# Optimization experiments

Hardware: AMD Instinct MI355X
Metric: run time of the kernel (lower is better)

## Reference

```python
import jax, jax.numpy as jnp
import numpy as np

N_NODES = 50000
N_EDGES = 800000
VOCAB = 500
IN_DIM = 128
HID = 128
OUT_DIM = 64
N_GRAPHS = 512


def setup_inputs() -> dict:
    key = jax.random.key(0)
    ks = jax.random.split(key, 12)
    s = 0.05
    return {
        "emb": jax.random.normal(ks[0], (VOCAB, IN_DIM), jnp.float32) * s,
        "w1a": jax.random.normal(ks[1], (HID, IN_DIM), jnp.float32) * s,
        "b1a": jnp.zeros((HID,), jnp.float32),
        "w1b": jax.random.normal(ks[2], (HID, HID), jnp.float32) * s,
        "b1b": jnp.zeros((HID,), jnp.float32),
        "w2a": jax.random.normal(ks[3], (HID, HID), jnp.float32) * s,
        "b2a": jnp.zeros((HID,), jnp.float32),
        "w2b": jax.random.normal(ks[4], (HID, HID), jnp.float32) * s,
        "b2b": jnp.zeros((HID,), jnp.float32),
        "fc_w": jax.random.normal(ks[5], (OUT_DIM, HID), jnp.float32) * s,
        "fc_b": jnp.zeros((OUT_DIM,), jnp.float32),
        "x_idx": jax.random.randint(ks[6], (N_NODES,), 0, VOCAB, jnp.int32),
        "edge_index": jax.random.randint(ks[7], (2, N_EDGES), 0, N_NODES, jnp.int32),
        "batch": jnp.sort(jax.random.randint(ks[8], (N_NODES,), 0, N_GRAPHS, jnp.int32)),
    }


def gin_conv(x, wa, ba, wb, bb, src, dst):
    # GINConv with eps=0: MLP(x + sum_{j->i} x_j)
    agg = jax.ops.segment_sum(x[src], dst, num_segments=N_NODES)  # [N, d]
    h = x + agg
    h = jax.nn.relu(h @ wa.T + ba)
    return h @ wb.T + bb


def reference(emb, w1a, b1a, w1b, b1b, w2a, b2a, w2b, b2b, fc_w, fc_b,
              x_idx, edge_index, batch):
    src, dst = edge_index[0], edge_index[1]
    x = emb[x_idx]  # [N, IN_DIM] embedding lookup
    x = jax.nn.relu(gin_conv(x, w1a, b1a, w1b, b1b, src, dst))
    x = jax.nn.relu(gin_conv(x, w2a, b2a, w2b, b2b, src, dst))
    # global mean pool over graphs
    sums = jax.ops.segment_sum(x, batch, num_segments=N_GRAPHS)  # [G, HID]
    cnt = jax.ops.segment_sum(jnp.ones((N_NODES,), x.dtype), batch, num_segments=N_GRAPHS)
    pooled = sums / jnp.maximum(cnt, 1.0)[:, None]
    return pooled @ fc_w.T + fc_b  # [G, OUT_DIM]
```

## Files before the change

kernel.cpp:

```cpp
#include <hip/hip_runtime.h>

#define N_NODES 50000
#define N_EDGES 800000
#define DIM 128
#define NGRAPH 512
#define ODIM 64
#define VOCAB 500
#define NBKT 391
#define NB2 128
#define EPB2 (N_EDGES / NB2)
#define CAP 4096

typedef __attribute__((ext_vector_type(8))) short bf16x8;
typedef __attribute__((ext_vector_type(4))) short bf16x4;
typedef __attribute__((ext_vector_type(4))) float f32x4;

__device__ inline unsigned short f2bf(float f) {
  unsigned u = __builtin_bit_cast(unsigned, f);
  return (unsigned short)((u + 0x7fffu + ((u >> 16) & 1u)) >> 16);
}
__device__ inline float bf2f(unsigned short h) {
  unsigned u = ((unsigned)h) << 16;
  return __builtin_bit_cast(float, u);
}

__global__ __launch_bounds__(256) void prep_kernel(
    const float* __restrict__ emb,
    const float* __restrict__ w1a, const float* __restrict__ w1b,
    const float* __restrict__ w2a, const float* __restrict__ w2b,
    unsigned short* __restrict__ embb, unsigned short* __restrict__ wbf,
    int* __restrict__ gcnt) {
  int u = blockIdx.x * 256 + threadIdx.x;
  if (u < NBKT) gcnt[u] = 0;
  const float* src;
  unsigned short* dst;
  if (u < VOCAB * 16) {
    src = emb + (size_t)u * 8;
    dst = embb + (size_t)u * 8;
  } else {
    int v = u - VOCAB * 16;
    if (v >= 4 * 2048) return;
    int m = v >> 11, loc = v & 2047;
    const float* w = (m == 0) ? w1a : (m == 1) ? w1b : (m == 2) ? w2a : w2b;
    src = w + (size_t)loc * 8;
    dst = wbf + (size_t)v * 8;
  }
  f32x4 a = ((const f32x4*)src)[0], b = ((const f32x4*)src)[1];
  bf16x8 o;
  #pragma unroll
  for (int e = 0; e < 4; ++e) {
    o[e] = (short)f2bf(a[e]);
    o[4 + e] = (short)f2bf(b[e]);
  }
  *(bf16x8*)dst = o;
}

__global__ __launch_bounds__(512) void build_kernel(
    const int* __restrict__ ei, int* __restrict__ gcnt,
    unsigned* __restrict__ eb) {
  __shared__ unsigned cnt[NBKT];
  __shared__ unsigned base[NBKT];
  int t = threadIdx.x, b = blockIdx.x;
  for (int i = t; i < NBKT; i += 512) cnt[i] = 0;
  __syncthreads();
  int ebase = b * EPB2;
  for (int i = t; i < EPB2; i += 512)
    atomicAdd(&cnt[(unsigned)ei[N_EDGES + ebase + i] >> 7], 1u);
  __syncthreads();
  for (int i = t; i < NBKT; i += 512) {
    base[i] = (unsigned)atomicAdd(&gcnt[i], (int)cnt[i]);
    cnt[i] = 0;
  }
  __syncthreads();
  for (int i = t; i < EPB2; i += 512) {
    int sn = ei[ebase + i];
    unsigned d = (unsigned)ei[N_EDGES + ebase + i];
    unsigned bk = d >> 7;
    unsigned r = atomicAdd(&cnt[bk], 1u);
    unsigned pos = base[bk] + r;
    if (pos < CAP)
      eb[(size_t)bk * CAP + pos] = ((d & 127u) << 16) | (unsigned)sn;
  }
}

__global__ __launch_bounds__(512) void sort_agg1_kernel(
    const unsigned* __restrict__ eb, const int* __restrict__ gcnt,
    const unsigned short* __restrict__ embb, const int* __restrict__ xidx,
    unsigned short* __restrict__ srt16, int* __restrict__ rowlo,
    int* __restrict__ rowhi, unsigned short* __restrict__ xa) {
  __shared__ unsigned stage[CAP];
  __shared__ unsigned short sorted[CAP];
  __shared__ unsigned hist[128], cur[128];
  __shared__ unsigned wtot;
  int t = threadIdx.x, bkt = blockIdx.x;
  int cnt = gcnt[bkt];
  if (cnt > CAP) cnt = CAP;
  size_t ebbase = (size_t)bkt * CAP;
  if (t < 128) hist[t] = 0;
  __syncthreads();
  for (int i = t; i < cnt; i += 512) {
    unsigned e = eb[ebbase + i];
    stage[i] = e;
    atomicAdd(&hist[e >> 16], 1u);
  }
  __syncthreads();
  if (t < 128) {
    int lane = t & 63;
    unsigned v = hist[t], ss = v;
    #pragma unroll
    for (int d = 1; d < 64; d <<= 1) {
      unsigned u = __shfl_up(ss, d, 64);
      if (lane >= d) ss += u;
    }
    if (t == 63) wtot = ss;
    cur[t] = ss - v;
  }
  __syncthreads();
  if (t < 128) {
    unsigned e0 = cur[t] + (t >= 64 ? wtot : 0u);
    cur[t] = e0;
    int n = bkt * 128 + t;
    if (n < N_NODES) {
      rowlo[n] = (int)(ebbase + e0);
      rowhi[n] = (int)(ebbase + e0 + hist[t]);
    }
  }
  __syncthreads();
  for (int i = t; i < cnt; i += 512) {
    unsigned e = stage[i];
    unsigned r = atomicAdd(&cur[e >> 16], 1u);
    sorted[r] = (unsigned short)(e & 0xFFFFu);
  }
  __syncthreads();

  for (int i = t; i < cnt; i += 512) srt16[ebbase + i] = sorted[i];

  int g = t >> 4, c = t & 15;
  for (int ii = 0; ii < 4; ++ii) {
    int dloc = ii * 32 + g;
    int node = bkt * 128 + dloc;
    if (node >= N_NODES) continue;
    int hi = (int)cur[dloc];
    int lo = hi - (int)hist[dloc];
    bf16x8 sv = *(const bf16x8*)(embb + (size_t)xidx[node] * DIM + c * 8);
    float a[8];
    #pragma unroll
    for (int e = 0; e < 8; ++e) a[e] = bf2f((unsigned short)sv[e]);
    int k = lo;
    for (; k + 8 <= hi; k += 8) {
      bf16x8 w[8];
      #pragma unroll
      for (int q = 0; q < 8; ++q)
        w[q] = *(const bf16x8*)(embb + (size_t)xidx[sorted[k + q]] * DIM + c * 8);
      #pragma unroll
      for (int q = 0; q < 8; ++q)
        #pragma unroll
        for (int e = 0; e < 8; ++e) a[e] += bf2f((unsigned short)w[q][e]);
    }
    for (; k + 2 <= hi; k += 2) {
      bf16x8 w0 = *(const bf16x8*)(embb + (size_t)xidx[sorted[k]] * DIM + c * 8);
      bf16x8 w1 = *(const bf16x8*)(embb + (size_t)xidx[sorted[k + 1]] * DIM + c * 8);
      #pragma unroll
      for (int e = 0; e < 8; ++e)
        a[e] += bf2f((unsigned short)w0[e]) + bf2f((unsigned short)w1[e]);
    }
    if (k < hi) {
      bf16x8 w = *(const bf16x8*)(embb + (size_t)xidx[sorted[k]] * DIM + c * 8);
      #pragma unroll
      for (int e = 0; e < 8; ++e) a[e] += bf2f((unsigned short)w[e]);
    }
    bf16x8 o;
    #pragma unroll
    for (int e = 0; e < 8; ++e) o[e] = (short)f2bf(a[e]);
    *(bf16x8*)(xa + (size_t)node * DIM + c * 8) = o;
  }
}

__global__ __launch_bounds__(256) void agg_x_kernel(
    const unsigned short* __restrict__ x, const int* __restrict__ rowlo,
    const int* __restrict__ rowhi, const unsigned short* __restrict__ srt16,
    unsigned short* __restrict__ xa) {
  int n = blockIdx.x * 16 + (threadIdx.x >> 4);
  int c = threadIdx.x & 15;
  int lo = rowlo[n], hi = rowhi[n];
  bf16x8 sv = *(const bf16x8*)(x + (size_t)n * DIM + c * 8);
  float a[8];
  #pragma unroll
  for (int e = 0; e < 8; ++e) a[e] = bf2f((unsigned short)sv[e]);
  int k = lo;
  for (; k + 8 <= hi; k += 8) {
    bf16x8 w[8];
    #pragma unroll
    for (int q = 0; q < 8; ++q)
      w[q] = *(const bf16x8*)(x + (size_t)srt16[k + q] * DIM + c * 8);
    #pragma unroll
    for (int q = 0; q < 8; ++q)
      #pragma unroll
      for (int e = 0; e < 8; ++e) a[e] += bf2f((unsigned short)w[q][e]);
  }
  for (; k + 2 <= hi; k += 2) {
    bf16x8 w0 = *(const bf16x8*)(x + (size_t)srt16[k] * DIM + c * 8);
    bf16x8 w1 = *(const bf16x8*)(x + (size_t)srt16[k + 1] * DIM + c * 8);
    #pragma unroll
    for (int e = 0; e < 8; ++e)
      a[e] += bf2f((unsigned short)w0[e]) + bf2f((unsigned short)w1[e]);
  }
  if (k < hi) {
    bf16x8 w = *(const bf16x8*)(x + (size_t)srt16[k] * DIM + c * 8);
    #pragma unroll
    for (int e = 0; e < 8; ++e) a[e] += bf2f((unsigned short)w[e]);
  }
  bf16x8 o;
  #pragma unroll
  for (int e = 0; e < 8; ++e) o[e] = (short)f2bf(a[e]);
  *(bf16x8*)(xa + (size_t)n * DIM + c * 8) = o;
}

__global__ __launch_bounds__(256) void mlp_mfma_kernel(
    const unsigned short* __restrict__ xa,
    const unsigned short* __restrict__ wabf, const float* __restrict__ ba,
    const unsigned short* __restrict__ wbbf, const float* __restrict__ bb,
    unsigned short* __restrict__ xout) {
  __shared__ short Xs[64 * 128];
  __shared__ short Hs[64 * 128];
  int t = threadIdx.x;
  int lane = t & 63;
  int w = t >> 6;
  int jq = w * 32;
  int l15 = lane & 15;
  int lg = lane >> 4;

  bf16x8 waf[2][4], wbf[2][4];
  #pragma unroll
  for (int jm = 0; jm < 2; ++jm) {
    int jrow = jq + jm * 16 + l15;
    #pragma unroll
    for (int ks = 0; ks < 4; ++ks) {
      int k0 = ks * 32 + lg * 8;
      waf[jm][ks] = *(const bf16x8*)(wabf + (size_t)jrow * DIM + k0);
      wbf[jm][ks] = *(const bf16x8*)(wbbf + (size_t)jrow * DIM + k0);
    }
  }
  f32x4 ba_r[2], bb_r[2];
  #pragma unroll
  for (int jm = 0; jm < 2; ++jm) {
    ba_r[jm] = *(const f32x4*)(ba + jq + jm * 16 + lg * 4);
    bb_r[jm] = *(const f32x4*)(bb + jq + jm * 16 + lg * 4);
  }

  for (int half = 0; half < 2; ++half) {
    int nbase = blockIdx.x * 128 + half * 64;

    {
      int r = t >> 2;
      int cb = (t & 3) * 4;
      int node = nbase + r;
      #pragma unroll
      for (int i = 0; i < 4; ++i) {
        int chunk = cb + i;
        bf16x8 v = {0, 0, 0, 0, 0, 0, 0, 0};
        if (node < N_NODES)
          v = *(const bf16x8*)(xa + (size_t)node * DIM + chunk * 8);
        *(bf16x8*)&Xs[r * 128 + ((chunk ^ (r & 7)) << 3)] = v;
      }
    }
    __syncthreads();

    #pragma unroll
    for (int nt = 0; nt < 4; ++nt) {
      int rrow = nt * 16 + l15;
      bf16x8 xf[4];
      #pragma unroll
      for (int ks = 0; ks < 4; ++ks) {
        int chunk = ks * 4 + lg;
        xf[ks] = *(const bf16x8*)&Xs[rrow * 128 + ((chunk ^ (rrow & 7)) << 3)];
      }
      #pragma unroll
      for (int jm = 0; jm < 2; ++jm) {
        f32x4 acc = ba_r[jm];
        #pragma unroll
        for (int ks = 0; ks < 4; ++ks)
          acc = __builtin_amdgcn_mfma_f32_16x16x32_bf16(waf[jm][ks], xf[ks], acc, 0, 0, 0);
        int hnode = nt * 16 + l15;
        int cbase = jq + jm * 16 + lg * 4;
        unsigned p0 = (unsigned)f2bf(fmaxf(acc[0], 0.f)) |
                      ((unsigned)f2bf(fmaxf(acc[1], 0.f)) << 16);
        unsigned p1 = (unsigned)f2bf(fmaxf(acc[2], 0.f)) |
                      ((unsigned)f2bf(fmaxf(acc[3], 0.f)) << 16);
        unsigned idx = hnode * 128 + (((cbase >> 3) ^ (hnode & 7)) << 3) + (cbase & 7);
        *(uint2*)&Hs[idx] = make_uint2(p0, p1);
      }
    }
    __syncthreads();

    #pragma unroll
    for (int nt = 0; nt < 4; ++nt) {
      int rrow = nt * 16 + l15;
      bf16x8 hf[4];
      #pragma unroll
      for (int ks = 0; ks < 4; ++ks) {
        int chunk = ks * 4 + lg;
        hf[ks] = *(const bf16x8*)&Hs[rrow * 128 + ((chunk ^ (rrow & 7)) << 3)];
      }
      #pragma unroll
      for (int jm = 0; jm < 2; ++jm) {
        f32x4 acc = bb_r[jm];
        #pragma unroll
        for (int ks = 0; ks < 4; ++ks)
          acc = __builtin_amdgcn_mfma_f32_16x16x32_bf16(wbf[jm][ks], hf[ks], acc, 0, 0, 0);
        int node = nbase + nt * 16 + l15;
        if (node < N_NODES) {
          bf16x4 o;
          #pragma unroll
          for (int e = 0; e < 4; ++e) o[e] = (short)f2bf(fmaxf(acc[e], 0.f));
          *(bf16x4*)(xout + (size_t)node * DIM + jq + jm * 16 + lg * 4) = o;
        }
      }
    }
    __syncthreads();
  }
}

#define PP 132
__global__ __launch_bounds__(256) void pool_fc_kernel(
    const unsigned short* __restrict__ x, const int* __restrict__ batch,
    const float* __restrict__ fcw, const float* __restrict__ fcb,
    float* __restrict__ out) {
  int g = blockIdx.x, t = threadIdx.x;
  __shared__ float part[16 * PP];
  __shared__ float pooled[DIM];
  __shared__ int sbound[2];
  if (t < 2) {
    int target = g + t;
    int lo = 0, hi = N_NODES;
    while (lo < hi) {
      int m = (lo + hi) >> 1;
      if (batch[m] < target) lo = m + 1; else hi = m;
    }
    sbound[t] = lo;
  }
  __syncthreads();
  int lo = sbound[0], hi = sbound[1];
  int r = t >> 4, c = t & 15;
  float acc[8] = {0.f, 0.f, 0.f, 0.f, 0.f, 0.f, 0.f, 0.f};
  for (int nn = lo + r; nn < hi; nn += 16) {
    bf16x8 v = *(const bf16x8*)(x + (size_t)nn * DIM + c * 8);
    #pragma unroll
    for (int e = 0; e < 8; ++e) acc[e] += bf2f((unsigned short)v[e]);
  }
  #pragma unroll
  for (int e = 0; e < 8; ++e) part[r * PP + c * 8 + e] = acc[e];
  __syncthreads();
  if (t < DIM) {
    float s = 0.f;
    #pragma unroll
    for (int rr = 0; rr < 16; ++rr) s += part[rr * PP + t];
    pooled[t] = s / fmaxf((float)(hi - lo), 1.0f);
  }
  __syncthreads();
  if (t < ODIM) {
    float a = fcb[t];
    const float* wr = fcw + (size_t)t * DIM;
    #pragma unroll 8
    for (int h = 0; h < DIM; ++h) a += pooled[h] * wr[h];
    out[(size_t)g * ODIM + t] = a;
  }
}

extern "C" void kernel_launch(void* const* d_in, const int* in_sizes, int n_in,
                              void* d_out, int out_size, void* d_ws, size_t ws_size,
                              hipStream_t stream) {
  const float* emb  = (const float*)d_in[0];
  const float* w1a  = (const float*)d_in[1];
  const float* b1a  = (const float*)d_in[2];
  const float* w1b  = (const float*)d_in[3];
  const float* b1b  = (const float*)d_in[4];
  const float* w2a  = (const float*)d_in[5];
  const float* b2a  = (const float*)d_in[6];
  const float* w2b  = (const float*)d_in[7];
  const float* b2b  = (const float*)d_in[8];
  const float* fcw  = (const float*)d_in[9];
  const float* fcb  = (const float*)d_in[10];
  const int*   xidx = (const int*)d_in[11];
  const int*   ei   = (const int*)d_in[12];
  const int*   batch= (const int*)d_in[13];
  float* out = (float*)d_out;

  size_t featb = (size_t)N_NODES * DIM * sizeof(unsigned short);
  char* ws = (char*)d_ws;
  unsigned short* B1 = (unsigned short*)ws;
  unsigned short* B2 = (unsigned short*)(ws + featb);
  char* p = ws + 2 * featb;
  unsigned short* embb = (unsigned short*)p;  p += (VOCAB * DIM * 2 + 15) / 16 * 16;
  unsigned short* wbf  = (unsigned short*)p;  p += (4 * DIM * DIM * 2 + 15) / 16 * 16;
  int* gcnt  = (int*)p;     p += (NBKT * 4 + 15) / 16 * 16;
  int* rowlo = (int*)p;     p += ((size_t)N_NODES * 4 + 15) / 16 * 16;
  int* rowhi = (int*)p;     p += ((size_t)N_NODES * 4 + 15) / 16 * 16;
  unsigned* eb = (unsigned*)p;          p += (size_t)NBKT * CAP * 4;
  unsigned short* srt16 = (unsigned short*)p;

  const unsigned short* w1abf = wbf;
  const unsigned short* w1bbf = wbf + DIM * DIM;
  const unsigned short* w2abf = wbf + 2 * DIM * DIM;
  const unsigned short* w2bbf = wbf + 3 * DIM * DIM;

  prep_kernel<<<(VOCAB * 16 + 4 * 2048 + 255) / 256, 256, 0, stream>>>(
      emb, w1a, w1b, w2a, w2b, embb, wbf, gcnt);

  build_kernel<<<NB2, 512, 0, stream>>>(ei, gcnt, eb);

  sort_agg1_kernel<<<NBKT, 512, 0, stream>>>(eb, gcnt, embb, xidx, srt16, rowlo, rowhi, B1);
  mlp_mfma_kernel<<<(N_NODES + 127) / 128, 256, 0, stream>>>(B1, w1abf, b1a, w1bbf, b1b, B2);

  agg_x_kernel<<<N_NODES / 16, 256, 0, stream>>>(B2, rowlo, rowhi, srt16, B1);
  mlp_mfma_kernel<<<(N_NODES + 127) / 128, 256, 0, stream>>>(B1, w2abf, b2a, w2bbf, b2b, B2);

  pool_fc_kernel<<<NGRAPH, 256, 0, stream>>>(B2, batch, fcw, fcb, out);
}
```

Measured before the change: 120.6 us.

## Fuse global mean-pool into second MLP kernel and widen sort/agg blocks

The second GIN MLP kernel now writes its ReLU output into shared memory as fp32 and accumulates per-graph column sums straight into a global pooled buffer with atomics. This skips writing and re-reading the final node features, and the pool kernel becomes a small FC kernel that divides by the node count. The sort/aggregate kernel also moves from 512 to 1024 threads per block so each thread handles fewer destination nodes. The cost is float atomics (non-deterministic summation order), a 64KB shared buffer that may lower occupancy, and an extra zeroing pass in prep.

```diff
diff --git a/kernel.cpp b/kernel.cpp
--- a/kernel.cpp
+++ b/kernel.cpp
@@ -29,9 +29,10 @@
     const float* __restrict__ w1a, const float* __restrict__ w1b,
     const float* __restrict__ w2a, const float* __restrict__ w2b,
     unsigned short* __restrict__ embb, unsigned short* __restrict__ wbf,
-    int* __restrict__ gcnt) {
+    int* __restrict__ gcnt, float* __restrict__ pooled) {
   int u = blockIdx.x * 256 + threadIdx.x;
   if (u < NBKT) gcnt[u] = 0;
+  for (int i = u; i < NGRAPH * DIM; i += 64 * 256) pooled[i] = 0.f;
   const float* src;
   unsigned short* dst;
   if (u < VOCAB * 16) {
@@ -83,7 +84,7 @@
   }
 }
 
-__global__ __launch_bounds__(512) void sort_agg1_kernel(
+__global__ __launch_bounds__(1024) void sort_agg1_kernel(
     const unsigned* __restrict__ eb, const int* __restrict__ gcnt,
     const unsigned short* __restrict__ embb, const int* __restrict__ xidx,
     unsigned short* __restrict__ srt16, int* __restrict__ rowlo,
@@ -98,7 +99,7 @@
   size_t ebbase = (size_t)bkt * CAP;
   if (t < 128) hist[t] = 0;
   __syncthreads();
-  for (int i = t; i < cnt; i += 512) {
+  for (int i = t; i < cnt; i += 1024) {
     unsigned e = eb[ebbase + i];
     stage[i] = e;
     atomicAdd(&hist[e >> 16], 1u);
@@ -126,18 +127,18 @@
     }
   }
   __syncthreads();
-  for (int i = t; i < cnt; i += 512) {
+  for (int i = t; i < cnt; i += 1024) {
     unsigned e = stage[i];
     unsigned r = atomicAdd(&cur[e >> 16], 1u);
     sorted[r] = (unsigned short)(e & 0xFFFFu);
   }
   __syncthreads();
 
-  for (int i = t; i < cnt; i += 512) srt16[ebbase + i] = sorted[i];
+  for (int i = t; i < cnt; i += 1024) srt16[ebbase + i] = sorted[i];
 
   int g = t >> 4, c = t & 15;
-  for (int ii = 0; ii < 4; ++ii) {
-    int dloc = ii * 32 + g;
+  for (int ii = 0; ii < 2; ++ii) {
+    int dloc = ii * 64 + g;
     int node = bkt * 128 + dloc;
     if (node >= N_NODES) continue;
     int hi = (int)cur[dloc];
@@ -216,13 +217,17 @@
   *(bf16x8*)(xa + (size_t)n * DIM + c * 8) = o;
 }
 
+template <int POOL>
 __global__ __launch_bounds__(256) void mlp_mfma_kernel(
     const unsigned short* __restrict__ xa,
     const unsigned short* __restrict__ wabf, const float* __restrict__ ba,
     const unsigned short* __restrict__ wbbf, const float* __restrict__ bb,
-    unsigned short* __restrict__ xout) {
-  __shared__ short Xs[64 * 128];
-  __shared__ short Hs[64 * 128];
+    unsigned short* __restrict__ xout, const int* __restrict__ batch,
+    float* __restrict__ pooled) {
+  __shared__ char smem[65536];
+  short* Xs = (short*)smem;
+  short* Hs = (short*)(smem + 32768);
+  float* Fs = (float*)smem;
   int t = threadIdx.x;
   int lane = t & 63;
   int w = t >> 6;
@@ -266,6 +271,7 @@
     }
     __syncthreads();
 
+    f32x4 acc2[4][2];
     #pragma unroll
     for (int nt = 0; nt < 4; ++nt) {
       int rrow = nt * 16 + l15;
@@ -308,28 +314,60 @@
         #pragma unroll
         for (int ks = 0; ks < 4; ++ks)
           acc = __builtin_amdgcn_mfma_f32_16x16x32_bf16(wbf[jm][ks], hf[ks], acc, 0, 0, 0);
-        int node = nbase + nt * 16 + l15;
-        if (node < N_NODES) {
-          bf16x4 o;
+        if (POOL == 0) {
+          int node = nbase + rrow;
+          if (node < N_NODES) {
+            bf16x4 o;
+            #pragma unroll
+            for (int e = 0; e < 4; ++e) o[e] = (short)f2bf(fmaxf(acc[e], 0.f));
+            *(bf16x4*)(xout + (size_t)node * DIM + jq + jm * 16 + lg * 4) = o;
+          }
+        } else {
+          acc2[nt][jm] = acc;
+        }
+      }
+    }
+
+    if (POOL == 1) {
+      __syncthreads();
+      #pragma unroll
+      for (int nt = 0; nt < 4; ++nt) {
+        int rrow = nt * 16 + l15;
+        #pragma unroll
+        for (int jm = 0; jm < 2; ++jm) {
+          int cbase = jq + jm * 16 + lg * 4;
           #pragma unroll
-          for (int e = 0; e < 4; ++e) o[e] = (short)f2bf(fmaxf(acc[e], 0.f));
-          *(bf16x4*)(xout + (size_t)node * DIM + jq + jm * 16 + lg * 4) = o;
+          for (int e = 0; e < 4; ++e)
+            Fs[rrow * 128 + cbase + e] = fmaxf(acc2[nt][jm][e], 0.f);
         }
       }
+      __syncthreads();
+      int d = t & 127;
+      int h = t >> 7;
+      float s = 0.f;
+      int curg = -1;
+      for (int nn = h * 32; nn < h * 32 + 32; ++nn) {
+        int node = nbase + nn;
+        if (node >= N_NODES) break;
+        int gg = batch[node];
+        if (gg != curg) {
+          if (curg >= 0 && s != 0.f) atomicAdd(&pooled[curg * DIM + d], s);
+          curg = gg; s = 0.f;
+        }
+        s += Fs[nn * 128 + d];
+      }
+      if (curg >= 0 && s != 0.f) atomicAdd(&pooled[curg * DIM + d], s);
     }
     __syncthreads();
   }
 }
 
-#define PP 132
-__global__ __launch_bounds__(256) void pool_fc_kernel(
-    const unsigned short* __restrict__ x, const int* __restrict__ batch,
+__global__ __launch_bounds__(64) void fc_kernel(
+    const float* __restrict__ pooled, const int* __restrict__ batch,
     const float* __restrict__ fcw, const float* __restrict__ fcb,
     float* __restrict__ out) {
   int g = blockIdx.x, t = threadIdx.x;
-  __shared__ float part[16 * PP];
-  __shared__ float pooled[DIM];
-  __shared__ int sbound[2];
+  __shared__ int sb[2];
   if (t < 2) {
     int target = g + t;
     int lo = 0, hi = N_NODES;
@@ -337,34 +375,16 @@
       int m = (lo + hi) >> 1;
       if (batch[m] < target) lo = m + 1; else hi = m;
     }
-    sbound[t] = lo;
-  }
-  __syncthreads();
-  int lo = sbound[0], hi = sbound[1];
-  int r = t >> 4, c = t & 15;
-  float acc[8] = {0.f, 0.f, 0.f, 0.f, 0.f, 0.f, 0.f, 0.f};
-  for (int nn = lo + r; nn < hi; nn += 16) {
-    bf16x8 v = *(const bf16x8*)(x + (size_t)nn * DIM + c * 8);
-    #pragma unroll
-    for (int e = 0; e < 8; ++e) acc[e] += bf2f((unsigned short)v[e]);
-  }
-  #pragma unroll
-  for (int e = 0; e < 8; ++e) part[r * PP + c * 8 + e] = acc[e];
-  __syncthreads();
-  if (t < DIM) {
-    float s = 0.f;
-    #pragma unroll
-    for (int rr = 0; rr < 16; ++rr) s += part[rr * PP + t];
-    pooled[t] = s / fmaxf((float)(hi - lo), 1.0f);
-  }
-  __syncthreads();
-  if (t < ODIM) {
-    float a = fcb[t];
-    const float* wr = fcw + (size_t)t * DIM;
-    #pragma unroll 8
-    for (int h = 0; h < DIM; ++h) a += pooled[h] * wr[h];
-    out[(size_t)g * ODIM + t] = a;
-  }
+    sb[t] = lo;
+  }
+  __syncthreads();
+  float inv = 1.f / fmaxf((float)(sb[1] - sb[0]), 1.0f);
+  float a = fcb[t];
+  const float* pr = pooled + (size_t)g * DIM;
+  const float* wr = fcw + (size_t)t * DIM;
+  #pragma unroll 8
+  for (int h = 0; h < DIM; ++h) a += pr[h] * inv * wr[h];
+  out[(size_t)g * ODIM + t] = a;
 }
 
 extern "C" void kernel_launch(void* const* d_in, const int* in_sizes, int n_in,
@@ -396,6 +416,7 @@
   int* gcnt  = (int*)p;     p += (NBKT * 4 + 15) / 16 * 16;
   int* rowlo = (int*)p;     p += ((size_t)N_NODES * 4 + 15) / 16 * 16;
   int* rowhi = (int*)p;     p += ((size_t)N_NODES * 4 + 15) / 16 * 16;
+  float* pooled = (float*)p; p += (size_t)NGRAPH * DIM * 4;
   unsigned* eb = (unsigned*)p;          p += (size_t)NBKT * CAP * 4;
   unsigned short* srt16 = (unsigned short*)p;
 
@@ -405,15 +426,17 @@
   const unsigned short* w2bbf = wbf + 3 * DIM * DIM;
 
   prep_kernel<<<(VOCAB * 16 + 4 * 2048 + 255) / 256, 256, 0, stream>>>(
-      emb, w1a, w1b, w2a, w2b, embb, wbf, gcnt);
+      emb, w1a, w1b, w2a, w2b, embb, wbf, gcnt, pooled);
 
   build_kernel<<<NB2, 512, 0, stream>>>(ei, gcnt, eb);
 
-  sort_agg1_kernel<<<NBKT, 512, 0, stream>>>(eb, gcnt, embb, xidx, srt16, rowlo, rowhi, B1);
-  mlp_mfma_kernel<<<(N_NODES + 127) / 128, 256, 0, stream>>>(B1, w1abf, b1a, w1bbf, b1b, B2);
+  sort_agg1_kernel<<<NBKT, 1024, 0, stream>>>(eb, gcnt, embb, xidx, srt16, rowlo, rowhi, B1);
+  mlp_mfma_kernel<0><<<(N_NODES + 127) / 128, 256, 0, stream>>>(
+      B1, w1abf, b1a, w1bbf, b1b, B2, batch, pooled);
 
   agg_x_kernel<<<N_NODES / 16, 256, 0, stream>>>(B2, rowlo, rowhi, srt16, B1);
-  mlp_mfma_kernel<<<(N_NODES + 127) / 128, 256, 0, stream>>>(B1, w2abf, b2a, w2bbf, b2b, B2);
-
-  pool_fc_kernel<<<NGRAPH, 256, 0, stream>>>(B2, batch, fcw, fcb, out);
-}
+  mlp_mfma_kernel<1><<<(N_NODES + 127) / 128, 256, 0, stream>>>(
+      B1, w2abf, b2a, w2bbf, b2b, nullptr, batch, pooled);
+
+  fc_kernel<<<NGRAPH, 64, 0, stream>>>(pooled, batch, fcw, fcb, out);
+}
```

Result: slower. 128.0 us (+6.1%).
